# Kernel tuning notes

Hardware: AMD Instinct MI355X
Metric: run time of the kernel (lower is better)

Reference implementation:

```python
import jax, jax.numpy as jnp
import numpy as np

EMBED_DIM = 1024
NUM_HEADS = 16
HEAD_DIM = EMBED_DIM // NUM_HEADS
ROPE_BASE = 10000.0


def setup_inputs() -> dict:
    key = jax.random.key(0)
    ks = jax.random.split(key, 9)
    B, S, E = 2, 2048, EMBED_DIM
    scale = 1.0 / np.sqrt(E)
    x = jax.random.normal(ks[0], (B, S, E), dtype=jnp.float32)
    Wq = jax.random.normal(ks[1], (E, E), dtype=jnp.float32) * scale
    bq = jnp.zeros((E,), dtype=jnp.float32)
    Wk = jax.random.normal(ks[2], (E, E), dtype=jnp.float32) * scale
    bk = jnp.zeros((E,), dtype=jnp.float32)
    Wv = jax.random.normal(ks[3], (E, E), dtype=jnp.float32) * scale
    bv = jnp.zeros((E,), dtype=jnp.float32)
    Wo = jax.random.normal(ks[4], (E, E), dtype=jnp.float32) * scale
    bo = jnp.zeros((E,), dtype=jnp.float32)
    return {"x": x, "Wq": Wq, "bq": bq, "Wk": Wk, "bk": bk,
            "Wv": Wv, "bv": bv, "Wo": Wo, "bo": bo}


def _rotary_emb(seq_len, dtype=jnp.float32):
    half = HEAD_DIM // 2
    inv_freq = 1.0 / (ROPE_BASE ** (jnp.arange(half, dtype=dtype) / half))
    pos = jnp.arange(seq_len, dtype=dtype)
    sinusoid = pos[:, None] * inv_freq[None, :]  # [S, half]
    sin = jnp.sin(sinusoid)
    cos = jnp.cos(sinusoid)
    # interleave-duplicate: (s0,s0,s1,s1,...) -> [S, HEAD_DIM]
    sin = jnp.stack((sin, sin), axis=-1).reshape(seq_len, HEAD_DIM)
    cos = jnp.stack((cos, cos), axis=-1).reshape(seq_len, HEAD_DIM)
    return sin, cos


def _rotate_half(x):
    x1 = x[..., ::2]
    x2 = x[..., 1::2]
    return jnp.stack((-x2, x1), axis=-1).reshape(x.shape)


def _apply_rope(x, sin, cos):
    # x: [B, H, S, D]; sin/cos: [S, D]
    return x * cos[None, None] + _rotate_half(x) * sin[None, None]


def reference(x, Wq, bq, Wk, bk, Wv, bv, Wo, bo):
    B, S, E = x.shape
    H, D = NUM_HEADS, HEAD_DIM

    def proj(W, b):
        t = x @ W.T + b  # [B, S, E]
        return t.reshape(B, S, H, D).transpose(0, 2, 1, 3)  # [B, H, S, D]

    q = proj(Wq, bq)
    k = proj(Wk, bk)
    v = proj(Wv, bv)

    sin, cos = _rotary_emb(S, x.dtype)
    q = _apply_rope(q, sin, cos)
    k = _apply_rope(k, sin, cos)

    scores = jnp.einsum("bhqd,bhkd->bhqk", q, k) / jnp.sqrt(jnp.asarray(D, x.dtype))
    causal = jnp.tril(jnp.ones((S, S), dtype=bool))  # keep lower triangle
    scores = jnp.where(causal[None, None], scores, -jnp.inf)
    weights = jax.nn.softmax(scores, axis=-1)
    out = jnp.einsum("bhqk,bhkd->bhqd", weights, v)
    out = out.transpose(0, 2, 1, 3).reshape(B, S, E)
    return out @ Wo.T + bo
```

## Files before the change

kernel.cpp:

```cpp
#include <hip/hip_runtime.h>
#include <hip/hip_bf16.h>
#include <cstdint>
#include <cstddef>

typedef __hip_bfloat16 bf16;
typedef __attribute__((ext_vector_type(8))) short bf16x8;
typedef __attribute__((ext_vector_type(4))) float f32x4;
typedef __attribute__((ext_vector_type(16))) float f32x16;

#define AS1C(p) ((const __attribute__((address_space(1))) void*)(p))
#define AS3(p)  ((__attribute__((address_space(3))) void*)(p))

constexpr int B_ = 2, S_ = 2048, E_ = 1024, H_ = 16, D_ = 64;
constexpr int M_ = B_ * S_;
constexpr float QSCALE_ = 0.125f * 1.44269504088896340736f;

__device__ __forceinline__ void gload_lds16(const bf16* g, bf16* l) {
  __builtin_amdgcn_global_load_lds(AS1C(g), AS3(l), 16, 0, 0);
}

__device__ __forceinline__ void cast4(const float* __restrict__ in, bf16* __restrict__ out, int i) {
  float4 v = reinterpret_cast<const float4*>(in)[i];
  union { bf16 b[4]; short4 s; } u;
  u.b[0] = __float2bfloat16(v.x);
  u.b[1] = __float2bfloat16(v.y);
  u.b[2] = __float2bfloat16(v.z);
  u.b[3] = __float2bfloat16(v.w);
  reinterpret_cast<short4*>(out)[i] = u.s;
}

__global__ void prep_kernel(const float* __restrict__ x,
                            const float* __restrict__ Wq, const float* __restrict__ Wk,
                            const float* __restrict__ Wv, const float* __restrict__ Wo,
                            const float* __restrict__ bq, const float* __restrict__ bk,
                            const float* __restrict__ bv,
                            bf16* __restrict__ xb, bf16* __restrict__ Wqkvb,
                            bf16* __restrict__ Wob, float* __restrict__ bqkv,
                            float* __restrict__ sintab, float* __restrict__ costab) {
  const int b = blockIdx.x, t = threadIdx.x;
  if (b < 4096) {
    cast4(x, xb, b * 256 + t);
  } else if (b < 5120) {
    cast4(Wo, Wob, (b - 4096) * 256 + t);
  } else if (b < 8192) {
    const int i = (b - 5120) * 256 + t;
    const int which = i >> 18;
    const int j = i & ((1 << 18) - 1);
    const float* src = which == 0 ? Wq : (which == 1 ? Wk : Wv);
    cast4(src, Wqkvb + (size_t)which * E_ * E_, j);
  } else if (b < 8448) {
    const int idx = (b - 8192) * 256 + t;
    const int s = idx >> 5, i = idx & 31;
    float inv = powf(10000.0f, -(float)i / 32.0f);
    float ang = (float)s * inv;
    sintab[idx] = sinf(ang);
    costab[idx] = cosf(ang);
  } else {
    for (int j = t; j < 768; j += 256) {
      const int which = j >> 8, jj = j & 255;
      const float* src = which == 0 ? bq : (which == 1 ? bk : bv);
      reinterpret_cast<float4*>(bqkv)[j] = reinterpret_cast<const float4*>(src)[jj];
    }
  }
}

__global__ __launch_bounds__(256)
void gemm_qkv(const bf16* __restrict__ A, const bf16* __restrict__ W,
              const float* __restrict__ bias,
              bf16* __restrict__ Qo, bf16* __restrict__ Ko, bf16* __restrict__ Vo,
              const float* __restrict__ sintab, const float* __restrict__ costab)
{
  constexpr int K = 1024, BK = 32;
  __shared__ __align__(16) bf16 smem[128 * 136];
  bf16* As = smem;
  bf16* Bs = smem + 128 * 32;
  const int tid = threadIdx.x;
  const int lane = tid & 63, wid = tid >> 6;
  const int g = lane >> 4, r16 = lane & 15;
  const int wr = wid >> 1, wc = wid & 1;

  const int nwg = gridDim.x * gridDim.y;
  const int flat = blockIdx.y * gridDim.x + blockIdx.x;
  const int cpx = nwg >> 3;
  const int f2 = (flat & 7) * cpx + (flat >> 3);
  const int m0 = (f2 / gridDim.x) * 128, n0 = (f2 % gridDim.x) * 128;

  const f32x4 fz = {0.f, 0.f, 0.f, 0.f};
  f32x4 acc[4][4];
#pragma unroll
  for (int mi = 0; mi < 4; ++mi)
#pragma unroll
    for (int ni = 0; ni < 4; ++ni) acc[mi][ni] = fz;

  const bf16* Abase = A + (size_t)m0 * K;
  const bf16* Wbase = W + (size_t)n0 * K;
  const int c0 = tid, c1 = 256 + tid;

  for (int k0 = 0; k0 < K; k0 += BK) {
    __syncthreads();
    gload_lds16(Abase + (size_t)(c0 >> 2) * K + k0 + (c0 & 3) * 8, As + c0 * 8);
    gload_lds16(Abase + (size_t)(c1 >> 2) * K + k0 + (c1 & 3) * 8, As + c1 * 8);
    gload_lds16(Wbase + (size_t)(c0 >> 2) * K + k0 + (c0 & 3) * 8, Bs + c0 * 8);
    gload_lds16(Wbase + (size_t)(c1 >> 2) * K + k0 + (c1 & 3) * 8, Bs + c1 * 8);
    __syncthreads();

    bf16x8 af[4], bfr[4];
#pragma unroll
    for (int mi = 0; mi < 4; ++mi)
      af[mi] = *reinterpret_cast<const bf16x8*>(As + (wr * 64 + mi * 16 + r16) * BK + 8 * g);
#pragma unroll
    for (int ni = 0; ni < 4; ++ni)
      bfr[ni] = *reinterpret_cast<const bf16x8*>(Bs + (wc * 64 + ni * 16 + r16) * BK + 8 * g);
    __builtin_amdgcn_s_setprio(1);
#pragma unroll
    for (int mi = 0; mi < 4; ++mi)
#pragma unroll
      for (int ni = 0; ni < 4; ++ni)
        acc[mi][ni] = __builtin_amdgcn_mfma_f32_16x16x32_bf16(af[mi], bfr[ni], acc[mi][ni], 0, 0, 0);
    __builtin_amdgcn_s_setprio(0);
  }

  const int b = m0 >> 11;
  if (n0 >= 2048) {
    __syncthreads();
#pragma unroll
    for (int mi = 0; mi < 4; ++mi) {
#pragma unroll
      for (int ni = 0; ni < 4; ++ni) {
        const int n_local = wc * 64 + ni * 16 + r16;
        const float bv = bias[n0 + n_local];
        const int m_base = wr * 64 + mi * 16 + g * 4;
        union { bf16 b4[4]; short4 s4; } u;
#pragma unroll
        for (int r = 0; r < 4; ++r) u.b4[r] = __float2bfloat16(acc[mi][ni][r] + bv);
        *reinterpret_cast<short4*>(&smem[n_local * 136 + m_base]) = u.s4;
      }
    }
    __syncthreads();
    const int srow0 = m0 & (S_ - 1);
#pragma unroll
    for (int i = 0; i < 8; ++i) {
      const int c = i * 256 + tid;
      const int row = c >> 4, cc = c & 15;
      const bf16x8 v = *reinterpret_cast<const bf16x8*>(&smem[row * 136 + cc * 8]);
      const int n = n0 + row;
      const int h = (n >> 6) & 15, d = n & 63;
      *reinterpret_cast<bf16x8*>(&Vo[((size_t)(b * H_ + h) * D_ + d) * S_ + srow0 + cc * 8]) = v;
    }
  } else {
#pragma unroll
    for (int mi = 0; mi < 4; ++mi) {
#pragma unroll
      for (int ni = 0; ni < 4; ++ni) {
        const int gn = n0 + wc * 64 + ni * 16 + r16;
        const float bv = bias[gn];
#pragma unroll
        for (int r = 0; r < 4; ++r) {
          const int gm = m0 + wr * 64 + mi * 16 + g * 4 + r;
          float val = acc[mi][ni][r] + bv;
          const int d = gn & 63;
          const int srow = gm & (S_ - 1);
          const float cs = costab[srow * 32 + (d >> 1)];
          const float sn = sintab[srow * 32 + (d >> 1)];
          const float pv = __shfl_xor(val, 1);
          val = (d & 1) ? (val * cs + pv * sn) : (val * cs - pv * sn);
          const int h = (gn >> 6) & 15;
          const size_t bh = (size_t)(b * H_ + h);
          if (gn < 1024) {
            Qo[(bh * S_ + srow) * D_ + d] = __float2bfloat16(val * QSCALE_);
          } else {
            Ko[(bh * S_ + srow) * D_ + d] = __float2bfloat16(val);
          }
        }
      }
    }
  }
}

__global__ __launch_bounds__(256)
void gemm_o(const bf16* __restrict__ A, const bf16* __restrict__ W,
            const float* __restrict__ bias, float* __restrict__ outF)
{
  constexpr int K = 1024, BK = 32;
  __shared__ __align__(16) bf16 As[64 * BK];
  __shared__ __align__(16) bf16 Bs[128 * BK];
  const int tid = threadIdx.x;
  const int lane = tid & 63;
  const int wc = tid >> 6;
  const int g = lane >> 4, r16 = lane & 15;

  const int flat = blockIdx.x;
  const int f2 = (flat & 7) * 64 + (flat >> 3);
  const int m0 = (f2 >> 3) * 64, n0 = (f2 & 7) * 128;

  const f32x4 fz = {0.f, 0.f, 0.f, 0.f};
  f32x4 acc[4][2];
#pragma unroll
  for (int mi = 0; mi < 4; ++mi)
#pragma unroll
    for (int ni = 0; ni < 2; ++ni) acc[mi][ni] = fz;

  const bf16* Abase = A + (size_t)m0 * K;
  const bf16* Wbase = W + (size_t)n0 * K;
  const int c0 = tid, c1 = 256 + tid;

  for (int k0 = 0; k0 < K; k0 += BK) {
    __syncthreads();
    gload_lds16(Abase + (size_t)(c0 >> 2) * K + k0 + (c0 & 3) * 8, As + c0 * 8);
    gload_lds16(Wbase + (size_t)(c0 >> 2) * K + k0 + (c0 & 3) * 8, Bs + c0 * 8);
    gload_lds16(Wbase + (size_t)(c1 >> 2) * K + k0 + (c1 & 3) * 8, Bs + c1 * 8);
    __syncthreads();

    bf16x8 af[4], bfr[2];
#pragma unroll
    for (int mi = 0; mi < 4; ++mi)
      af[mi] = *reinterpret_cast<const bf16x8*>(As + (mi * 16 + r16) * BK + 8 * g);
#pragma unroll
    for (int ni = 0; ni < 2; ++ni)
      bfr[ni] = *reinterpret_cast<const bf16x8*>(Bs + (wc * 32 + ni * 16 + r16) * BK + 8 * g);
    __builtin_amdgcn_s_setprio(1);
#pragma unroll
    for (int mi = 0; mi < 4; ++mi)
#pragma unroll
      for (int ni = 0; ni < 2; ++ni)
        acc[mi][ni] = __builtin_amdgcn_mfma_f32_16x16x32_bf16(af[mi], bfr[ni], acc[mi][ni], 0, 0, 0);
    __builtin_amdgcn_s_setprio(0);
  }

#pragma unroll
  for (int mi = 0; mi < 4; ++mi)
#pragma unroll
    for (int ni = 0; ni < 2; ++ni) {
      const int gn = n0 + wc * 32 + ni * 16 + r16;
      const float bv = bias[gn];
#pragma unroll
      for (int r = 0; r < 4; ++r) {
        const int gm = m0 + mi * 16 + g * 4 + r;
        outF[(size_t)gm * 1024 + gn] = acc[mi][ni][r] + bv;
      }
    }
}

__global__ __launch_bounds__(256)
void attn_kernel(const bf16* __restrict__ Q, const bf16* __restrict__ Kg,
                 const bf16* __restrict__ Vtg, bf16* __restrict__ Og)
{
  __shared__ __align__(16) bf16 Ks[2][2][64 * 64];
  __shared__ __align__(16) bf16 Vs[2][2][64 * 64];
  const int flat = blockIdx.x;
  const int bh = flat & 31;
  const int qblk = 31 - (flat >> 5);
  const int tid = threadIdx.x, lane = tid & 63, wid = tid >> 6;
  const int qg = wid & 1, ksl = wid >> 1;
  const int l31 = lane & 31, h = lane >> 5;
  const bf16* Qb = Q + (size_t)bh * S_ * D_;
  const bf16* Kb = Kg + (size_t)bh * S_ * D_;
  const bf16* Vb = Vtg + (size_t)bh * D_ * S_;
  const int b = bh >> 4, hd = bh & 15;
  bf16* Ob = Og + (size_t)b * S_ * E_ + hd * D_;

  const int q0 = qblk * 64;
  const int qw0 = q0 + qg * 32;
  const int nkt = qblk + 1;
  const int nsup = (nkt + 1) >> 1;

  bf16x8 qf[4];
#pragma unroll
  for (int i = 0; i < 4; ++i)
    qf[i] = *reinterpret_cast<const bf16x8*>(Qb + (size_t)(qw0 + l31) * 64 + 16 * i + 8 * h);

  f32x16 oacc0 = {};
  f32x16 oacc1 = {};
  float mrow = -__builtin_inff();
  float lrow = 0.f;

  auto stagepair = [&](int jp, int dbuf) {
    const int t0 = 2 * jp;
#pragma unroll
    for (int i = 0; i < 4; ++i) {
      const int kc = tid + 256 * i;
      const int tile = kc >> 9, c2 = kc & 511, r = c2 >> 3, cc = c2 & 7;
      gload_lds16(Kb + (size_t)((t0 + tile) * 64 + r) * 64 + ((cc ^ (r & 7)) * 8),
                  &Ks[dbuf][tile][c2 * 8]);
    }
#pragma unroll
    for (int i = 0; i < 4; ++i) {
      const int kc = tid + 256 * i;
      const int tile = kc >> 9, c2 = kc & 511, r = c2 >> 3, cc = c2 & 7;
      gload_lds16(Vb + (size_t)r * S_ + (t0 + tile) * 64 + ((cc ^ (r & 7)) * 8),
                  &Vs[dbuf][tile][c2 * 8]);
    }
  };

  stagepair(0, 0);
  __syncthreads();
  int cur = 0;

  for (int j = 0; j < nsup; ++j) {
    if (j + 1 < nsup) stagepair(j + 1, cur ^ 1);

    const int kt = 2 * j + ksl;
    if (kt < nkt) {
      const int k0 = kt * 64;
      if (k0 <= qw0 + 31) {
        const bf16* ksp = Ks[cur][ksl];
        const bf16* vsp = Vs[cur][ksl];
        f32x16 ps0 = {}, ps1 = {};
        __builtin_amdgcn_s_setprio(1);
#pragma unroll
        for (int i = 0; i < 4; ++i) {
          const bf16x8 ka0 = *reinterpret_cast<const bf16x8*>(
              &ksp[l31 * 64 + (((2 * i + h) ^ (l31 & 7)) * 8)]);
          ps0 = __builtin_amdgcn_mfma_f32_32x32x16_bf16(ka0, qf[i], ps0, 0, 0, 0);
        }
#pragma unroll
        for (int i = 0; i < 4; ++i) {
          const int row1 = 32 + l31;
          const bf16x8 ka1 = *reinterpret_cast<const bf16x8*>(
              &ksp[row1 * 64 + (((2 * i + h) ^ (row1 & 7)) * 8)]);
          ps1 = __builtin_amdgcn_mfma_f32_32x32x16_bf16(ka1, qf[i], ps1, 0, 0, 0);
        }
        __builtin_amdgcn_s_setprio(0);
        if (k0 + 63 > qw0) {
          const int qm = qw0 + l31 - k0;
#pragma unroll
          for (int r = 0; r < 16; ++r) {
            const int kl = (r & 3) + 8 * (r >> 2) + 4 * h;
            if (kl > qm) ps0[r] = -1e30f;
            if (32 + kl > qm) ps1[r] = -1e30f;
          }
        }
        float tm = ps0[0];
#pragma unroll
        for (int r = 1; r < 16; ++r) tm = fmaxf(tm, ps0[r]);
#pragma unroll
        for (int r = 0; r < 16; ++r) tm = fmaxf(tm, ps1[r]);
        tm = fmaxf(tm, __shfl_xor(tm, 32));
        if (__any((tm - mrow > 8.f) ? 1 : 0)) {
          const float mn = fmaxf(mrow, tm);
          const float scl = exp2f(mrow - mn);
          mrow = mn;
          lrow *= scl;
          float so[16];
#pragma unroll
          for (int r = 0; r < 16; ++r)
            so[r] = __shfl(scl, (r & 3) + 8 * (r >> 2) + 4 * h);
#pragma unroll
          for (int r = 0; r < 16; ++r) { oacc0[r] *= so[r]; oacc1[r] *= so[r]; }
        }
        float ssum = 0.f;
#pragma unroll
        for (int r = 0; r < 16; ++r) {
          const float p = exp2f(ps0[r] - mrow);
          ps0[r] = p; ssum += p;
        }
#pragma unroll
        for (int r = 0; r < 16; ++r) {
          const float p = exp2f(ps1[r] - mrow);
          ps1[r] = p; ssum += p;
        }
        lrow += ssum;
        unsigned int pk0[8], pk1[8];
#pragma unroll
        for (int i = 0; i < 8; ++i) {
          unsigned int r0, r1;
          asm("v_cvt_pk_bf16_f32 %0, %1, %2" : "=v"(r0) : "v"(ps0[2 * i]), "v"(ps0[2 * i + 1]));
          asm("v_cvt_pk_bf16_f32 %0, %1, %2" : "=v"(r1) : "v"(ps1[2 * i]), "v"(ps1[2 * i + 1]));
          pk0[i] = r0; pk1[i] = r1;
        }
#pragma unroll
        for (int ks = 0; ks < 4; ++ks) {
          const int ksq = ks & 1;
          unsigned int w0, w1, w2, w3;
          if (ks < 2) { w0 = pk0[4 * ksq]; w2 = pk0[4 * ksq + 2];
                        w1 = pk0[4 * ksq + 1]; w3 = pk0[4 * ksq + 3]; }
          else        { w0 = pk1[4 * ksq]; w2 = pk1[4 * ksq + 2];
                        w1 = pk1[4 * ksq + 1]; w3 = pk1[4 * ksq + 3]; }
          asm("v_permlane32_swap_b32 %0, %1" : "+v"(w0), "+v"(w2));
          asm("v_permlane32_swap_b32 %0, %1" : "+v"(w1), "+v"(w3));
          union { unsigned int w[4]; bf16x8 v; } A;
          A.w[0] = w0; A.w[1] = w1; A.w[2] = w2; A.w[3] = w3;
          const int sw = l31 & 7;
          const bf16x8 vf0 = *reinterpret_cast<const bf16x8*>(
              &vsp[l31 * 64 + (((2 * ks + h) ^ sw) * 8)]);
          const bf16x8 vf1 = *reinterpret_cast<const bf16x8*>(
              &vsp[(32 + l31) * 64 + (((2 * ks + h) ^ sw) * 8)]);
          __builtin_amdgcn_s_setprio(1);
          oacc0 = __builtin_amdgcn_mfma_f32_32x32x16_bf16(A.v, vf0, oacc0, 0, 0, 0);
          oacc1 = __builtin_amdgcn_mfma_f32_32x32x16_bf16(A.v, vf1, oacc1, 0, 0, 0);
          __builtin_amdgcn_s_setprio(0);
        }
      }
    }

    __syncthreads();
    cur ^= 1;
  }

  lrow += __shfl_xor(lrow, 32);

  float* Obuf = (float*)&Ks[0][0][0];
  float* mlb  = (float*)&Vs[0][0][0];
  if (ksl == 1) {
#pragma unroll
    for (int r = 0; r < 16; ++r) {
      const int crow = (r & 3) + 8 * (r >> 2) + 4 * h;
      Obuf[(qg * 32 + crow) * 64 + l31] = oacc0[r];
      Obuf[(qg * 32 + crow) * 64 + 32 + l31] = oacc1[r];
    }
    if (h == 0) {
      mlb[(qg * 32 + l31) * 2] = mrow;
      mlb[(qg * 32 + l31) * 2 + 1] = lrow;
    }
  }
  __syncthreads();
  if (ksl == 0) {
    const float pm = mlb[(qg * 32 + l31) * 2];
    const float pl = mlb[(qg * 32 + l31) * 2 + 1];
    const float mstar = fmaxf(mrow, pm);
    const float a = exp2f(mrow - mstar);
    const float bb = exp2f(pm - mstar);
    const float linv = 1.0f / (lrow * a + pl * bb);
    const float fa = a * linv, fb = bb * linv;
#pragma unroll
    for (int r = 0; r < 16; ++r) {
      const int crow = (r & 3) + 8 * (r >> 2) + 4 * h;
      const float far = __shfl(fa, crow);
      const float fbr = __shfl(fb, crow);
      const int qrow = qw0 + crow;
      const float o0 = oacc0[r] * far + Obuf[(qg * 32 + crow) * 64 + l31] * fbr;
      const float o1 = oacc1[r] * far + Obuf[(qg * 32 + crow) * 64 + 32 + l31] * fbr;
      Ob[(size_t)qrow * E_ + l31] = __float2bfloat16(o0);
      Ob[(size_t)qrow * E_ + 32 + l31] = __float2bfloat16(o1);
    }
  }
}

extern "C" void kernel_launch(void* const* d_in, const int* in_sizes, int n_in,
                              void* d_out, int out_size, void* d_ws, size_t ws_size,
                              hipStream_t stream) {
  const float* x  = (const float*)d_in[0];
  const float* Wq = (const float*)d_in[1];
  const float* bq = (const float*)d_in[2];
  const float* Wk = (const float*)d_in[3];
  const float* bk = (const float*)d_in[4];
  const float* Wv = (const float*)d_in[5];
  const float* bv = (const float*)d_in[6];
  const float* Wo = (const float*)d_in[7];
  const float* bo = (const float*)d_in[8];
  float* out = (float*)d_out;

  char* ws = (char*)d_ws;
  size_t off = 0;
  auto alloc = [&](size_t bytes) -> char* {
    char* p = ws + off; off += (bytes + 255) & ~(size_t)255; return p;
  };
  bf16* xb    = (bf16*)alloc((size_t)M_ * E_ * 2);
  bf16* Wqkvb = (bf16*)alloc((size_t)3 * E_ * E_ * 2);
  bf16* Wob   = (bf16*)alloc((size_t)E_ * E_ * 2);
  float* bqkv = (float*)alloc((size_t)3 * E_ * 4);
  bf16* Qb    = (bf16*)alloc((size_t)M_ * E_ * 2);
  bf16* Kb    = (bf16*)alloc((size_t)M_ * E_ * 2);
  bf16* Vtb   = (bf16*)alloc((size_t)M_ * E_ * 2);
  bf16* AOb   = (bf16*)alloc((size_t)M_ * E_ * 2);
  float* sintab = (float*)alloc((size_t)S_ * 32 * 4);
  float* costab = (float*)alloc((size_t)S_ * 32 * 4);

  prep_kernel<<<dim3(8449), 256, 0, stream>>>(x, Wq, Wk, Wv, Wo, bq, bk, bv,
                                              xb, Wqkvb, Wob, bqkv, sintab, costab);

  gemm_qkv<<<dim3(24, 32), 256, 0, stream>>>(xb, Wqkvb, bqkv, Qb, Kb, Vtb, sintab, costab);
  attn_kernel<<<dim3(1024), 256, 0, stream>>>(Qb, Kb, Vtb, AOb);
  gemm_o<<<dim3(512), 256, 0, stream>>>(AOb, Wob, bo, out);
}
```

Baseline: 125.5 us.

## Shrink QKV GEMM tile to 128x64, k-major LDS layout, staged Q/K stores

The QKV projection GEMM now uses 128x64 tiles launched as 1536 blocks instead of 768, which gives more workgroups to fill the GPU. Both GEMMs switch their LDS layout to k-chunk-major, so each fragment read is a contiguous 16-byte row slice and bank conflicts should drop. The Q/K epilogue now applies RoPE and writes the result through shared memory, then issues coalesced 16-byte stores instead of scattered 2-byte writes. The trade-off is less reuse of A per block, since the A tile is loaded twice as often overall.

```diff
diff --git a/kernel.cpp b/kernel.cpp
--- a/kernel.cpp
+++ b/kernel.cpp
@@ -71,65 +71,99 @@
               const float* __restrict__ sintab, const float* __restrict__ costab)
 {
   constexpr int K = 1024, BK = 32;
-  __shared__ __align__(16) bf16 smem[128 * 136];
+  __shared__ __align__(16) bf16 smem[9216];
   bf16* As = smem;
-  bf16* Bs = smem + 128 * 32;
+  bf16* Bs = smem + 4096;
   const int tid = threadIdx.x;
   const int lane = tid & 63, wid = tid >> 6;
-  const int g = lane >> 4, r16 = lane & 15;
+  const int gq = lane >> 4, r16 = lane & 15;
   const int wr = wid >> 1, wc = wid & 1;
 
-  const int nwg = gridDim.x * gridDim.y;
-  const int flat = blockIdx.y * gridDim.x + blockIdx.x;
-  const int cpx = nwg >> 3;
-  const int f2 = (flat & 7) * cpx + (flat >> 3);
-  const int m0 = (f2 / gridDim.x) * 128, n0 = (f2 % gridDim.x) * 128;
+  const int flat = blockIdx.x;
+  const int f2 = (flat & 7) * 192 + (flat >> 3);
+  const int mt = f2 / 48, nt = f2 % 48;
+  const int m0 = mt * 128, n0 = nt * 64;
 
   const f32x4 fz = {0.f, 0.f, 0.f, 0.f};
-  f32x4 acc[4][4];
+  f32x4 acc[4][2];
 #pragma unroll
   for (int mi = 0; mi < 4; ++mi)
 #pragma unroll
-    for (int ni = 0; ni < 4; ++ni) acc[mi][ni] = fz;
+    for (int ni = 0; ni < 2; ++ni) acc[mi][ni] = fz;
 
   const bf16* Abase = A + (size_t)m0 * K;
   const bf16* Wbase = W + (size_t)n0 * K;
-  const int c0 = tid, c1 = 256 + tid;
 
   for (int k0 = 0; k0 < K; k0 += BK) {
     __syncthreads();
-    gload_lds16(Abase + (size_t)(c0 >> 2) * K + k0 + (c0 & 3) * 8, As + c0 * 8);
-    gload_lds16(Abase + (size_t)(c1 >> 2) * K + k0 + (c1 & 3) * 8, As + c1 * 8);
-    gload_lds16(Wbase + (size_t)(c0 >> 2) * K + k0 + (c0 & 3) * 8, Bs + c0 * 8);
-    gload_lds16(Wbase + (size_t)(c1 >> 2) * K + k0 + (c1 & 3) * 8, Bs + c1 * 8);
-    __syncthreads();
-
-    bf16x8 af[4], bfr[4];
+    {
+      const int c0 = tid, c1 = 256 + tid;
+      gload_lds16(Abase + (size_t)(c0 & 127) * K + k0 + (c0 >> 7) * 8, As + c0 * 8);
+      gload_lds16(Abase + (size_t)(c1 & 127) * K + k0 + (c1 >> 7) * 8, As + c1 * 8);
+      gload_lds16(Wbase + (size_t)(tid & 63) * K + k0 + (tid >> 6) * 8, Bs + tid * 8);
+    }
+    __syncthreads();
+
+    bf16x8 af[4], bfr[2];
 #pragma unroll
     for (int mi = 0; mi < 4; ++mi)
-      af[mi] = *reinterpret_cast<const bf16x8*>(As + (wr * 64 + mi * 16 + r16) * BK + 8 * g);
-#pragma unroll
-    for (int ni = 0; ni < 4; ++ni)
-      bfr[ni] = *reinterpret_cast<const bf16x8*>(Bs + (wc * 64 + ni * 16 + r16) * BK + 8 * g);
+      af[mi] = *reinterpret_cast<const bf16x8*>(As + (gq * 128 + wr * 64 + mi * 16 + r16) * 8);
+#pragma unroll
+    for (int ni = 0; ni < 2; ++ni)
+      bfr[ni] = *reinterpret_cast<const bf16x8*>(Bs + (gq * 64 + wc * 32 + ni * 16 + r16) * 8);
     __builtin_amdgcn_s_setprio(1);
 #pragma unroll
     for (int mi = 0; mi < 4; ++mi)
 #pragma unroll
-      for (int ni = 0; ni < 4; ++ni)
+      for (int ni = 0; ni < 2; ++ni)
         acc[mi][ni] = __builtin_amdgcn_mfma_f32_16x16x32_bf16(af[mi], bfr[ni], acc[mi][ni], 0, 0, 0);
     __builtin_amdgcn_s_setprio(0);
   }
 
   const int b = m0 >> 11;
-  if (n0 >= 2048) {
-    __syncthreads();
+  __syncthreads();
+  if (n0 < 2048) {
 #pragma unroll
     for (int mi = 0; mi < 4; ++mi) {
 #pragma unroll
-      for (int ni = 0; ni < 4; ++ni) {
-        const int n_local = wc * 64 + ni * 16 + r16;
+      for (int ni = 0; ni < 2; ++ni) {
+        const int gn = n0 + wc * 32 + ni * 16 + r16;
+        const float bv = bias[gn];
+        const int d = gn & 63;
+#pragma unroll
+        for (int r = 0; r < 4; ++r) {
+          const int ml = wr * 64 + mi * 16 + gq * 4 + r;
+          const int srow = (m0 + ml) & (S_ - 1);
+          float val = acc[mi][ni][r] + bv;
+          const float cs = costab[srow * 32 + (d >> 1)];
+          const float sn = sintab[srow * 32 + (d >> 1)];
+          const float pv = __shfl_xor(val, 1);
+          val = (d & 1) ? (val * cs + pv * sn) : (val * cs - pv * sn);
+          if (n0 < 1024) val *= QSCALE_;
+          smem[ml * 72 + wc * 32 + ni * 16 + r16] = __float2bfloat16(val);
+        }
+      }
+    }
+    __syncthreads();
+    bf16* dstbase = (n0 < 1024 ? Qo : Ko);
+    const int h = (n0 >> 6) & 15;
+    const size_t bh = (size_t)(b * H_ + h);
+#pragma unroll
+    for (int i = 0; i < 4; ++i) {
+      const int c = i * 256 + tid;
+      const int row = c >> 3, cc = c & 7;
+      const bf16x8 v = *reinterpret_cast<const bf16x8*>(&smem[row * 72 + cc * 8]);
+      const int srow = (m0 + row) & (S_ - 1);
+      *reinterpret_cast<bf16x8*>(&dstbase[(bh * S_ + srow) * D_ + cc * 8]) = v;
+    }
+  } else {
+#pragma unroll
+    for (int mi = 0; mi < 4; ++mi) {
+#pragma unroll
+      for (int ni = 0; ni < 2; ++ni) {
+        const int n_local = wc * 32 + ni * 16 + r16;
         const float bv = bias[n0 + n_local];
-        const int m_base = wr * 64 + mi * 16 + g * 4;
+        const int m_base = wr * 64 + mi * 16 + gq * 4;
         union { bf16 b4[4]; short4 s4; } u;
 #pragma unroll
         for (int r = 0; r < 4; ++r) u.b4[r] = __float2bfloat16(acc[mi][ni][r] + bv);
@@ -139,40 +173,13 @@
     __syncthreads();
     const int srow0 = m0 & (S_ - 1);
 #pragma unroll
-    for (int i = 0; i < 8; ++i) {
+    for (int i = 0; i < 4; ++i) {
       const int c = i * 256 + tid;
       const int row = c >> 4, cc = c & 15;
       const bf16x8 v = *reinterpret_cast<const bf16x8*>(&smem[row * 136 + cc * 8]);
       const int n = n0 + row;
       const int h = (n >> 6) & 15, d = n & 63;
       *reinterpret_cast<bf16x8*>(&Vo[((size_t)(b * H_ + h) * D_ + d) * S_ + srow0 + cc * 8]) = v;
-    }
-  } else {
-#pragma unroll
-    for (int mi = 0; mi < 4; ++mi) {
-#pragma unroll
-      for (int ni = 0; ni < 4; ++ni) {
-        const int gn = n0 + wc * 64 + ni * 16 + r16;
-        const float bv = bias[gn];
-#pragma unroll
-        for (int r = 0; r < 4; ++r) {
-          const int gm = m0 + wr * 64 + mi * 16 + g * 4 + r;
-          float val = acc[mi][ni][r] + bv;
-          const int d = gn & 63;
-          const int srow = gm & (S_ - 1);
-          const float cs = costab[srow * 32 + (d >> 1)];
-          const float sn = sintab[srow * 32 + (d >> 1)];
-          const float pv = __shfl_xor(val, 1);
-          val = (d & 1) ? (val * cs + pv * sn) : (val * cs - pv * sn);
-          const int h = (gn >> 6) & 15;
-          const size_t bh = (size_t)(b * H_ + h);
-          if (gn < 1024) {
-            Qo[(bh * S_ + srow) * D_ + d] = __float2bfloat16(val * QSCALE_);
-          } else {
-            Ko[(bh * S_ + srow) * D_ + d] = __float2bfloat16(val);
-          }
-        }
-      }
     }
   }
 }
@@ -186,8 +193,8 @@
   __shared__ __align__(16) bf16 Bs[128 * BK];
   const int tid = threadIdx.x;
   const int lane = tid & 63;
-  const int wc = tid >> 6;
-  const int g = lane >> 4, r16 = lane & 15;
+  const int wcq = tid >> 6;
+  const int gq = lane >> 4, r16 = lane & 15;
 
   const int flat = blockIdx.x;
   const int f2 = (flat & 7) * 64 + (flat >> 3);
@@ -202,22 +209,24 @@
 
   const bf16* Abase = A + (size_t)m0 * K;
   const bf16* Wbase = W + (size_t)n0 * K;
-  const int c0 = tid, c1 = 256 + tid;
 
   for (int k0 = 0; k0 < K; k0 += BK) {
     __syncthreads();
-    gload_lds16(Abase + (size_t)(c0 >> 2) * K + k0 + (c0 & 3) * 8, As + c0 * 8);
-    gload_lds16(Wbase + (size_t)(c0 >> 2) * K + k0 + (c0 & 3) * 8, Bs + c0 * 8);
-    gload_lds16(Wbase + (size_t)(c1 >> 2) * K + k0 + (c1 & 3) * 8, Bs + c1 * 8);
+    {
+      gload_lds16(Abase + (size_t)(tid & 63) * K + k0 + (tid >> 6) * 8, As + tid * 8);
+      const int c0 = tid, c1 = 256 + tid;
+      gload_lds16(Wbase + (size_t)(c0 & 127) * K + k0 + (c0 >> 7) * 8, Bs + c0 * 8);
+      gload_lds16(Wbase + (size_t)(c1 & 127) * K + k0 + (c1 >> 7) * 8, Bs + c1 * 8);
+    }
     __syncthreads();
 
     bf16x8 af[4], bfr[2];
 #pragma unroll
     for (int mi = 0; mi < 4; ++mi)
-      af[mi] = *reinterpret_cast<const bf16x8*>(As + (mi * 16 + r16) * BK + 8 * g);
+      af[mi] = *reinterpret_cast<const bf16x8*>(As + (gq * 64 + mi * 16 + r16) * 8);
 #pragma unroll
     for (int ni = 0; ni < 2; ++ni)
-      bfr[ni] = *reinterpret_cast<const bf16x8*>(Bs + (wc * 32 + ni * 16 + r16) * BK + 8 * g);
+      bfr[ni] = *reinterpret_cast<const bf16x8*>(Bs + (gq * 128 + wcq * 32 + ni * 16 + r16) * 8);
     __builtin_amdgcn_s_setprio(1);
 #pragma unroll
     for (int mi = 0; mi < 4; ++mi)
@@ -231,11 +240,11 @@
   for (int mi = 0; mi < 4; ++mi)
 #pragma unroll
     for (int ni = 0; ni < 2; ++ni) {
-      const int gn = n0 + wc * 32 + ni * 16 + r16;
+      const int gn = n0 + wcq * 32 + ni * 16 + r16;
       const float bv = bias[gn];
 #pragma unroll
       for (int r = 0; r < 4; ++r) {
-        const int gm = m0 + mi * 16 + g * 4 + r;
+        const int gm = m0 + mi * 16 + gq * 4 + r;
         outF[(size_t)gm * 1024 + gn] = acc[mi][ni][r] + bv;
       }
     }
@@ -378,16 +387,16 @@
                         w1 = pk1[4 * ksq + 1]; w3 = pk1[4 * ksq + 3]; }
           asm("v_permlane32_swap_b32 %0, %1" : "+v"(w0), "+v"(w2));
           asm("v_permlane32_swap_b32 %0, %1" : "+v"(w1), "+v"(w3));
-          union { unsigned int w[4]; bf16x8 v; } A;
-          A.w[0] = w0; A.w[1] = w1; A.w[2] = w2; A.w[3] = w3;
+          union { unsigned int w[4]; bf16x8 v; } Aw;
+          Aw.w[0] = w0; Aw.w[1] = w1; Aw.w[2] = w2; Aw.w[3] = w3;
           const int sw = l31 & 7;
           const bf16x8 vf0 = *reinterpret_cast<const bf16x8*>(
               &vsp[l31 * 64 + (((2 * ks + h) ^ sw) * 8)]);
           const bf16x8 vf1 = *reinterpret_cast<const bf16x8*>(
               &vsp[(32 + l31) * 64 + (((2 * ks + h) ^ sw) * 8)]);
           __builtin_amdgcn_s_setprio(1);
-          oacc0 = __builtin_amdgcn_mfma_f32_32x32x16_bf16(A.v, vf0, oacc0, 0, 0, 0);
-          oacc1 = __builtin_amdgcn_mfma_f32_32x32x16_bf16(A.v, vf1, oacc1, 0, 0, 0);
+          oacc0 = __builtin_amdgcn_mfma_f32_32x32x16_bf16(Aw.v, vf0, oacc0, 0, 0, 0);
+          oacc1 = __builtin_amdgcn_mfma_f32_32x32x16_bf16(Aw.v, vf1, oacc1, 0, 0, 0);
           __builtin_amdgcn_s_setprio(0);
         }
       }
@@ -469,7 +478,7 @@
   prep_kernel<<<dim3(8449), 256, 0, stream>>>(x, Wq, Wk, Wv, Wo, bq, bk, bv,
                                               xb, Wqkvb, Wob, bqkv, sintab, costab);
 
-  gemm_qkv<<<dim3(24, 32), 256, 0, stream>>>(xb, Wqkvb, bqkv, Qb, Kb, Vtb, sintab, costab);
+  gemm_qkv<<<dim3(1536), 256, 0, stream>>>(xb, Wqkvb, bqkv, Qb, Kb, Vtb, sintab, costab);
   attn_kernel<<<dim3(1024), 256, 0, stream>>>(Qb, Kb, Vtb, AOb);
   gemm_o<<<dim3(512), 256, 0, stream>>>(AOb, Wob, bo, out);
 }
```

Measured after the change: 168.6 us. 34.4% more time.
